# Kernel tuning notes

Hardware: AMD Instinct MI355X
Metric: run time of the kernel (lower is better)

## Reference

```python
import jax, jax.numpy as jnp
import numpy as np

EMB = 1024
NH = 16
T = 2048
B = 2

def setup_inputs() -> dict:
    key = jax.random.key(0)
    k1, k2, k3, k4, k5 = jax.random.split(key, 5)
    s = 0.02
    return {
        "x": jax.random.normal(k1, (B, T, EMB), dtype=jnp.float32),
        "W_attn": jax.random.normal(k2, (EMB, 3 * EMB), dtype=jnp.float32) * s,
        "b_attn": jax.random.normal(k3, (3 * EMB,), dtype=jnp.float32) * s,
        "W_proj": jax.random.normal(k4, (EMB, EMB), dtype=jnp.float32) * s,
        "b_proj": jax.random.normal(k5, (EMB,), dtype=jnp.float32) * s,
    }

def reference(x, W_attn, b_attn, W_proj, b_proj):
    Bz, Tz, C = x.shape
    hd = C // NH
    qkv = x @ W_attn + b_attn                      # [B,T,3C]
    q, k, v = jnp.split(qkv, 3, axis=-1)
    # [B,T,C] -> [B,H,T,hd]
    def heads(t):
        return t.reshape(Bz, Tz, NH, hd).transpose(0, 2, 1, 3)
    q, k, v = heads(q), heads(k), heads(v)
    scale = 1.0 / jnp.sqrt(jnp.float32(hd))
    att = jnp.einsum("bhqd,bhkd->bhqk", q, k) * scale   # [B,H,T,T]
    causal = jnp.tril(jnp.ones((Tz, Tz), dtype=bool))
    att = jnp.where(causal, att, jnp.finfo(att.dtype).min)
    att = jax.nn.softmax(att, axis=-1)
    y = jnp.einsum("bhqk,bhkd->bhqd", att, v)            # [B,H,T,hd]
    y = y.transpose(0, 2, 1, 3).reshape(Bz, Tz, C)
    return y @ W_proj + b_proj
```

## Files before the change

### kernel.cpp

```cpp
#include <hip/hip_runtime.h>
#include <cstdint>
#include <cstddef>

typedef _Float16 half8 __attribute__((ext_vector_type(8)));
typedef _Float16 half4v __attribute__((ext_vector_type(4)));
typedef float f32x4 __attribute__((ext_vector_type(4)));
typedef int int4v __attribute__((ext_vector_type(4)));

#define EMBD 1024
#define NHEAD 16
#define TSEQ 2048
#define NB 2
#define HD 64
#define NBH (NB*NHEAD)
#define SCK 0.18033688f

static __device__ __forceinline__ void gload_lds16(const void* g, void* l) {
    __builtin_amdgcn_global_load_lds((const __attribute__((address_space(1))) void*)g,
                                     (__attribute__((address_space(3))) void*)l,
                                     16, 0, 0);
}

static __device__ __forceinline__ int pk2(float a, float b) {
    return __builtin_bit_cast(int, __builtin_amdgcn_cvt_pkrtz(a, b));
}

__global__ __launch_bounds__(256) void k_prep(
    const float* __restrict__ x,  _Float16* __restrict__ xh,
    const float* __restrict__ Wa, const float* __restrict__ Wp,
    _Float16* __restrict__ WaT,   _Float16* __restrict__ WpT)
{
    const int bx = blockIdx.x;
    if (bx < 4096) {
        int i = bx * 256 + threadIdx.x;
        float4 v = ((const float4*)x)[i];
        half4v h;
        h.x = (_Float16)v.x; h.y = (_Float16)v.y; h.z = (_Float16)v.z; h.w = (_Float16)v.w;
        ((half4v*)xh)[i] = h;
        return;
    }
    __shared__ float tile[32][33];
    const int idx = bx - 4096;
    const int bxx = idx & 127;
    const int byy = idx >> 7;
    const bool isA = bxx < 96;
    const float* in  = isA ? Wa : Wp;
    _Float16* out    = isA ? WaT : WpT;
    const int C      = isA ? 3072 : 1024;
    const int c0 = (isA ? bxx : bxx - 96) * 32, r0 = byy * 32;
    const int tx = threadIdx.x & 31, ty = threadIdx.x >> 5;
    #pragma unroll
    for (int j = 0; j < 4; ++j)
        tile[ty + 8*j][tx] = in[(size_t)(r0 + ty + 8*j) * C + c0 + tx];
    __syncthreads();
    #pragma unroll
    for (int j = 0; j < 4; ++j)
        out[(size_t)(c0 + ty + 8*j) * 1024 + r0 + tx] = (_Float16)tile[tx][ty + 8*j];
}

__global__ __launch_bounds__(512, 4) void k_gemm_qkv(
    const _Float16* __restrict__ A,
    const _Float16* __restrict__ Bt,
    const float* __restrict__ bias,
    _Float16* __restrict__ outq,
    _Float16* __restrict__ VT)
{
    __shared__ _Float16 smem[20480];
    _Float16* As = smem;

    const int d   = blockIdx.x;
    const int xcd = d & 7;
    const int idx = d >> 3;
    const int mt  = (xcd >> 1) * 8 + (idx & 7);
    const int ntl = (xcd &  1) * 8 + (idx >> 3);
    const int m0 = mt * 128;
    const int hc = ntl * 64;

    const int tid  = threadIdx.x;
    const int lane = tid & 63;
    const int w    = tid >> 6;
    const int wm   = w >> 2;
    const int wn   = w & 3;
    const int l15  = lane & 15;
    const int lg   = lane >> 4;

    f32x4 acc[4][3];
    #pragma unroll
    for (int i = 0; i < 4; ++i)
        #pragma unroll
        for (int j = 0; j < 3; ++j)
            acc[i][j] = (f32x4){0.f, 0.f, 0.f, 0.f};

    for (int kt = 0; kt < 16; ++kt) {
        __syncthreads();
        #pragma unroll
        for (int c = 0; c < 2; ++c) {
            int s = c * 512 + tid;
            int r = s >> 3, sl = s & 7;
            const _Float16* ga = A + (size_t)(m0 + r) * 1024 + kt * 64 + ((sl ^ (r & 7)) * 8);
            gload_lds16(ga, (char*)As + s * 16);
        }
        {
            int s = tid;
            int r = s >> 3, sl = s & 7;
            size_t goff = (size_t)(hc + r) * 1024 + kt * 64 + ((sl ^ (r & 7)) * 8);
            #pragma unroll
            for (int q = 0; q < 3; ++q)
                gload_lds16(Bt + goff + (size_t)q * 1024 * 1024,
                            (char*)(smem + 8192 + q * 4096) + s * 16);
        }
        __syncthreads();

        half8 af[4][2];
        #pragma unroll
        for (int mf = 0; mf < 4; ++mf) {
            int r = wm * 64 + mf * 16 + l15;
            #pragma unroll
            for (int ks = 0; ks < 2; ++ks)
                af[mf][ks] = *(const half8*)((const char*)As + r * 128 + (((ks * 4 + lg) ^ (r & 7)) * 16));
        }
        half8 bf[3][2];
        #pragma unroll
        for (int nf = 0; nf < 3; ++nf) {
            int nn = wn * 48 + nf * 16;
            const char* BsQ = (const char*)(smem + 8192 + (nn >> 6) * 4096);
            int r = (nn & 63) + l15;
            #pragma unroll
            for (int ks = 0; ks < 2; ++ks)
                bf[nf][ks] = *(const half8*)(BsQ + r * 128 + (((ks * 4 + lg) ^ (r & 7)) * 16));
        }
        #pragma unroll
        for (int mf = 0; mf < 4; ++mf)
            #pragma unroll
            for (int nf = 0; nf < 3; ++nf) {
                acc[mf][nf] = __builtin_amdgcn_mfma_f32_16x16x32_f16(af[mf][0], bf[nf][0], acc[mf][nf], 0, 0, 0);
                acc[mf][nf] = __builtin_amdgcn_mfma_f32_16x16x32_f16(af[mf][1], bf[nf][1], acc[mf][nf], 0, 0, 0);
            }
    }

    #pragma unroll
    for (int nf = 0; nf < 3; ++nf) {
        int nn = wn * 48 + nf * 16;
        int q  = nn >> 6;
        if (q < 2) {
            int col = (nn & 63) + l15;
            float bv = bias[q * 1024 + hc + col];
            float osc = (q == 1) ? SCK : 1.0f;
            #pragma unroll
            for (int mf = 0; mf < 4; ++mf) {
                #pragma unroll
                for (int j = 0; j < 4; ++j) {
                    int m = m0 + wm * 64 + mf * 16 + lg * 4 + j;
                    outq[(size_t)m * 3072 + q * 1024 + hc + col] = (_Float16)((acc[mf][nf][j] + bv) * osc);
                }
            }
        }
    }
    __syncthreads();
    #pragma unroll
    for (int nf = 0; nf < 3; ++nf) {
        int nn = wn * 48 + nf * 16;
        if ((nn >> 6) == 2) {
            int col = (nn & 63) + l15;
            float bv = bias[2048 + hc + col];
            #pragma unroll
            for (int mf = 0; mf < 4; ++mf) {
                #pragma unroll
                for (int j = 0; j < 4; ++j) {
                    int ml = wm * 64 + mf * 16 + lg * 4 + j;
                    smem[ml * 65 + col] = (_Float16)(acc[mf][nf][j] + bv);
                }
            }
        }
    }
    __syncthreads();

    {
        const int b     = m0 >> 11;
        const int tloc0 = m0 & 2047;
        _Float16* vbase = VT + ((size_t)(b * 16 + ntl) * 64) * 2048 + tloc0;
        #pragma unroll
        for (int c = 0; c < 2; ++c) {
            int seg = c * 512 + tid;
            int dd  = seg >> 4;
            int s   = seg & 15;
            half8 hv8;
            #pragma unroll
            for (int e = 0; e < 8; ++e) {
                int p = s * 8 + e;
                int k = 16 * (2 * (p >> 5) + ((p & 7) >> 2)) + 4 * ((p >> 3) & 3) + (p & 3);
                hv8[e] = smem[k * 65 + dd];
            }
            *(half8*)&vbase[(size_t)dd * 2048 + s * 8] = hv8;
        }
    }
}

__global__ __launch_bounds__(256) void k_gemm_proj(
    const _Float16* __restrict__ A,
    const _Float16* __restrict__ Bt,
    const float* __restrict__ bias,
    float* __restrict__ outf)
{
    __shared__ _Float16 As[64 * 64];
    __shared__ _Float16 Bs[128 * 64];

    const int d   = blockIdx.x;
    const int xcd = d & 7;
    const int idx = d >> 3;
    const int mt  = (xcd >> 1) * 16 + (idx & 15);
    const int nt  = (xcd &  1) * 4  + (idx >> 4);
    const int m0 = mt * 64, n0 = nt * 128;

    const int tid  = threadIdx.x;
    const int lane = tid & 63;
    const int wn   = tid >> 6;
    const int l15  = lane & 15;
    const int lg   = lane >> 4;

    f32x4 acc[4][2];
    #pragma unroll
    for (int i = 0; i < 4; ++i) {
        acc[i][0] = (f32x4){0.f, 0.f, 0.f, 0.f};
        acc[i][1] = (f32x4){0.f, 0.f, 0.f, 0.f};
    }

    for (int kt = 0; kt < 16; ++kt) {
        __syncthreads();
        #pragma unroll
        for (int c = 0; c < 2; ++c) {
            int s = c * 256 + tid;
            int r = s >> 3, sl = s & 7;
            const _Float16* ga = A + (size_t)(m0 + r) * 1024 + kt * 64 + ((sl ^ (r & 7)) * 8);
            gload_lds16(ga, (char*)As + s * 16);
        }
        #pragma unroll
        for (int c = 0; c < 4; ++c) {
            int s = c * 256 + tid;
            int r = s >> 3, sl = s & 7;
            const _Float16* gb = Bt + (size_t)(n0 + r) * 1024 + kt * 64 + ((sl ^ (r & 7)) * 8);
            gload_lds16(gb, (char*)Bs + s * 16);
        }
        __syncthreads();

        half8 af[4][2], bf[2][2];
        #pragma unroll
        for (int mf = 0; mf < 4; ++mf) {
            int r = mf * 16 + l15;
            #pragma unroll
            for (int ks = 0; ks < 2; ++ks)
                af[mf][ks] = *(const half8*)((const char*)As + r * 128 + (((ks * 4 + lg) ^ (r & 7)) * 16));
        }
        #pragma unroll
        for (int nf = 0; nf < 2; ++nf) {
            int r = wn * 32 + nf * 16 + l15;
            #pragma unroll
            for (int ks = 0; ks < 2; ++ks)
                bf[nf][ks] = *(const half8*)((const char*)Bs + r * 128 + (((ks * 4 + lg) ^ (r & 7)) * 16));
        }
        #pragma unroll
        for (int mf = 0; mf < 4; ++mf)
            #pragma unroll
            for (int nf = 0; nf < 2; ++nf) {
                acc[mf][nf] = __builtin_amdgcn_mfma_f32_16x16x32_f16(af[mf][0], bf[nf][0], acc[mf][nf], 0, 0, 0);
                acc[mf][nf] = __builtin_amdgcn_mfma_f32_16x16x32_f16(af[mf][1], bf[nf][1], acc[mf][nf], 0, 0, 0);
            }
    }

    float bv[2];
    bv[0] = bias[n0 + wn * 32 + l15];
    bv[1] = bias[n0 + wn * 32 + 16 + l15];

    #pragma unroll
    for (int mf = 0; mf < 4; ++mf) {
        #pragma unroll
        for (int j = 0; j < 4; ++j) {
            int m = m0 + mf * 16 + lg * 4 + j;
            float* po = outf + (size_t)m * 1024 + n0 + wn * 32 + l15;
            po[0]  = acc[mf][0][j] + bv[0];
            po[16] = acc[mf][1][j] + bv[1];
        }
    }
}

__global__ __launch_bounds__(512) void k_attn(
    const _Float16* __restrict__ qkv,
    const _Float16* __restrict__ VTg,
    _Float16* __restrict__ Y)
{
    __shared__ _Float16 Kt[2][8192];
    __shared__ _Float16 Vt[2][8192];

    const int tid  = threadIdx.x;
    const int lane = tid & 63;
    const int w    = tid >> 6;
    const int l15  = lane & 15;
    const int lg   = lane >> 4;
    const int bh   = blockIdx.x;
    const int by   = blockIdx.y;
    const int qt   = (by < 8) ? (15 - by) : (by - 8);
    const int b    = bh >> 4, h = bh & 15;

    const int rA  = tid >> 3;
    const int slA = tid & 7;
    const size_t kOffA = (size_t)rA * 3072 + ((slA ^ (rA & 7)) * 8);
    const _Float16* kBase = qkv + (size_t)(b * 2048) * 3072 + 1024 + h * 64;

    const int dA = tid >> 4;
    const int sA = tid & 15;
    const size_t vOffA = (size_t)dA * 2048 + ((sA ^ (dA & 15)) * 8);
    const _Float16* vBase = VTg + (size_t)bh * TSEQ * HD;

    const int x7   = l15 & 7;
    const int kph0 = (lg ^ x7) * 8;
    const int kph1 = ((4 + lg) ^ x7) * 8;

    const int qrow = qt * 128 + w * 16 + l15;
    const _Float16* qptr = qkv + (size_t)(b * 2048 + qrow) * 3072 + h * 64;
    half8 qa0 = *(const half8*)&qptr[lg * 8];
    half8 qa1 = *(const half8*)&qptr[32 + lg * 8];

    half8 ones;
    #pragma unroll
    for (int i = 0; i < 8; ++i) ones[i] = (_Float16)1.0f;

    f32x4 yac[4];
    #pragma unroll
    for (int nf = 0; nf < 4; ++nf) yac[nf] = (f32x4){0.f, 0.f, 0.f, 0.f};
    f32x4 lsum = (f32x4){0.f, 0.f, 0.f, 0.f};

    const int nkt = qt + 1;

    half8 kra = *(const half8*)(kBase + kOffA);
    half8 krb = *(const half8*)(kBase + kOffA + (size_t)64 * 3072);
    half8 vra = *(const half8*)(vBase + vOffA);
    half8 vrb = *(const half8*)(vBase + vOffA + 32 * 2048);

    for (int kt = 0; kt < nkt; ++kt) {
        const int cur = kt & 1;
        _Float16* KtC = Kt[cur];
        _Float16* VtC = Vt[cur];
        *(half8*)&KtC[tid * 8]        = kra;
        *(half8*)&KtC[4096 + tid * 8] = krb;
        *(half8*)&VtC[tid * 8]        = vra;
        *(half8*)&VtC[4096 + tid * 8] = vrb;
        if (kt + 1 < nkt) {
            const _Float16* kp = kBase + (size_t)(kt + 1) * 128 * 3072;
            kra = *(const half8*)(kp + kOffA);
            krb = *(const half8*)(kp + kOffA + (size_t)64 * 3072);
            const _Float16* vp = vBase + (kt + 1) * 128;
            vra = *(const half8*)(vp + vOffA);
            vrb = *(const half8*)(vp + vOffA + 32 * 2048);
        }
        asm volatile("s_waitcnt lgkmcnt(0)" ::: "memory");
        __builtin_amdgcn_s_barrier();
        __builtin_amdgcn_sched_barrier(0);

        const bool diag = (kt == nkt - 1);

        f32x4 s[8];
        __builtin_amdgcn_s_setprio(1);
        #pragma unroll
        for (int f = 0; f < 8; ++f) {
            if (diag && f > w) { s[f] = (f32x4){0.f, 0.f, 0.f, 0.f}; continue; }
            int rr = f * 16 + l15;
            half8 kb0 = *(const half8*)&KtC[rr * 64 + kph0];
            half8 kb1 = *(const half8*)&KtC[rr * 64 + kph1];
            f32x4 z = (f32x4){0.f, 0.f, 0.f, 0.f};
            z = __builtin_amdgcn_mfma_f32_16x16x32_f16(kb0, qa0, z, 0, 0, 0);
            z = __builtin_amdgcn_mfma_f32_16x16x32_f16(kb1, qa1, z, 0, 0, 0);
            s[f] = z;
        }
        __builtin_amdgcn_s_setprio(0);

        if (diag) {
            const int qg = qt * 128 + w * 16 + l15;
            #pragma unroll
            for (int f = 0; f < 8; ++f) {
                if (f > w) continue;
                #pragma unroll
                for (int j = 0; j < 4; ++j) {
                    int kk = kt * 128 + 16 * f + 4 * lg + j;
                    s[f][j] = (kk > qg) ? 0.f : exp2f(s[f][j]);
                }
            }
        } else {
            #pragma unroll
            for (int f = 0; f < 8; ++f)
                #pragma unroll
                for (int j = 0; j < 4; ++j) s[f][j] = exp2f(s[f][j]);
        }

        __builtin_amdgcn_s_setprio(1);
        #pragma unroll
        for (int t = 0; t < 4; ++t) {
            int4v pi;
            pi[0] = pk2(s[2 * t][0],     s[2 * t][1]);
            pi[1] = pk2(s[2 * t][2],     s[2 * t][3]);
            pi[2] = pk2(s[2 * t + 1][0], s[2 * t + 1][1]);
            pi[3] = pk2(s[2 * t + 1][2], s[2 * t + 1][3]);
            half8 pa = __builtin_bit_cast(half8, pi);
            lsum = __builtin_amdgcn_mfma_f32_16x16x32_f16(pa, ones, lsum, 0, 0, 0);
            #pragma unroll
            for (int nf = 0; nf < 4; ++nf) {
                half8 vb = *(const half8*)&VtC[(nf * 16 + l15) * 128 + (((t * 4 + lg) ^ l15) * 8)];
                yac[nf] = __builtin_amdgcn_mfma_f32_16x16x32_f16(pa, vb, yac[nf], 0, 0, 0);
            }
        }
        __builtin_amdgcn_s_setprio(0);
    }

    const int trow = qt * 128 + w * 16 + lg * 4;
    #pragma unroll
    for (int j = 0; j < 4; ++j) {
        float inv = 1.f / lsum[j];
        #pragma unroll
        for (int nf = 0; nf < 4; ++nf) {
            float yv = yac[nf][j] * inv;
            Y[((size_t)b * TSEQ + trow + j) * EMBD + h * 64 + nf * 16 + l15] = (_Float16)yv;
        }
    }
}

extern "C" void kernel_launch(void* const* d_in, const int* in_sizes, int n_in,
                              void* d_out, int out_size, void* d_ws, size_t ws_size,
                              hipStream_t stream) {
    const float* x  = (const float*)d_in[0];
    const float* Wa = (const float*)d_in[1];
    const float* ba = (const float*)d_in[2];
    const float* Wp = (const float*)d_in[3];
    const float* bp = (const float*)d_in[4];
    float* out = (float*)d_out;

    _Float16* Xh   = (_Float16*)d_ws;
    _Float16* WaT  = Xh   + (size_t)4096 * 1024;
    _Float16* WpT  = WaT  + (size_t)3072 * 1024;
    _Float16* QKVn = WpT  + (size_t)1024 * 1024;
    _Float16* VTb  = QKVn + (size_t)4096 * 3072;
    _Float16* Yh   = Xh;

    k_prep<<<8192, 256, 0, stream>>>(x, Xh, Wa, Wp, WaT, WpT);

    k_gemm_qkv<<<512, 512, 0, stream>>>(Xh, WaT, ba, QKVn, VTb);

    k_attn<<<dim3(NBH, 16), 512, 0, stream>>>(QKVn, VTb, Yh);

    k_gemm_proj<<<512, 256, 0, stream>>>(Yh, WpT, bp, out);
}
```

Before: 91.70 us.

## Halve attention block to 4 waves, each handling two 16-row query slices

The attention kernel now runs 256 threads per block instead of 512. Each wave processes two 16-row query fragments (rows w*16 and w*16+64) that share every K and V fragment loaded from LDS, so LDS read traffic per MFMA halves and each thread stages four K/V chunks instead of two. The diagonal-tile skip for fully masked fragments is dropped, so masked blocks are computed and then zeroed. The changes also raise register pressure, with launch bounds asking for two blocks per CU, and cut the number of waves available to hide latency.

```diff
diff --git a/kernel.cpp b/kernel.cpp
--- a/kernel.cpp
+++ b/kernel.cpp
@@ -283,7 +283,7 @@
     }
 }
 
-__global__ __launch_bounds__(512) void k_attn(
+__global__ __launch_bounds__(256, 2) void k_attn(
     const _Float16* __restrict__ qkv,
     const _Float16* __restrict__ VTg,
     _Float16* __restrict__ Y)
@@ -301,110 +301,145 @@
     const int qt   = (by < 8) ? (15 - by) : (by - 8);
     const int b    = bh >> 4, h = bh & 15;
 
-    const int rA  = tid >> 3;
-    const int slA = tid & 7;
-    const size_t kOffA = (size_t)rA * 3072 + ((slA ^ (rA & 7)) * 8);
+    const int sg0 = tid, sg1 = 256 + tid, sg2 = 512 + tid, sg3 = 768 + tid;
+    const size_t k0 = (size_t)(sg0 >> 3) * 3072 + (((sg0 & 7) ^ ((sg0 >> 3) & 7)) * 8);
+    const size_t k1 = (size_t)(sg1 >> 3) * 3072 + (((sg1 & 7) ^ ((sg1 >> 3) & 7)) * 8);
+    const size_t k2 = (size_t)(sg2 >> 3) * 3072 + (((sg2 & 7) ^ ((sg2 >> 3) & 7)) * 8);
+    const size_t k3 = (size_t)(sg3 >> 3) * 3072 + (((sg3 & 7) ^ ((sg3 >> 3) & 7)) * 8);
+    const size_t v0 = (size_t)(sg0 >> 4) * 2048 + (((sg0 & 15) ^ ((sg0 >> 4) & 15)) * 8);
+    const size_t v1 = (size_t)(sg1 >> 4) * 2048 + (((sg1 & 15) ^ ((sg1 >> 4) & 15)) * 8);
+    const size_t v2 = (size_t)(sg2 >> 4) * 2048 + (((sg2 & 15) ^ ((sg2 >> 4) & 15)) * 8);
+    const size_t v3 = (size_t)(sg3 >> 4) * 2048 + (((sg3 & 15) ^ ((sg3 >> 4) & 15)) * 8);
     const _Float16* kBase = qkv + (size_t)(b * 2048) * 3072 + 1024 + h * 64;
-
-    const int dA = tid >> 4;
-    const int sA = tid & 15;
-    const size_t vOffA = (size_t)dA * 2048 + ((sA ^ (dA & 15)) * 8);
     const _Float16* vBase = VTg + (size_t)bh * TSEQ * HD;
 
     const int x7   = l15 & 7;
     const int kph0 = (lg ^ x7) * 8;
     const int kph1 = ((4 + lg) ^ x7) * 8;
 
-    const int qrow = qt * 128 + w * 16 + l15;
-    const _Float16* qptr = qkv + (size_t)(b * 2048 + qrow) * 3072 + h * 64;
-    half8 qa0 = *(const half8*)&qptr[lg * 8];
-    half8 qa1 = *(const half8*)&qptr[32 + lg * 8];
+    const int qr0 = qt * 128 + w * 16 + l15;
+    const _Float16* qp0 = qkv + (size_t)(b * 2048 + qr0) * 3072 + h * 64;
+    const _Float16* qp1 = qp0 + (size_t)64 * 3072;
+    half8 qa0 = *(const half8*)&qp0[lg * 8];
+    half8 qa1 = *(const half8*)&qp0[32 + lg * 8];
+    half8 qa2 = *(const half8*)&qp1[lg * 8];
+    half8 qa3 = *(const half8*)&qp1[32 + lg * 8];
 
     half8 ones;
     #pragma unroll
     for (int i = 0; i < 8; ++i) ones[i] = (_Float16)1.0f;
 
-    f32x4 yac[4];
-    #pragma unroll
-    for (int nf = 0; nf < 4; ++nf) yac[nf] = (f32x4){0.f, 0.f, 0.f, 0.f};
-    f32x4 lsum = (f32x4){0.f, 0.f, 0.f, 0.f};
+    f32x4 yac0[4], yac1[4];
+    #pragma unroll
+    for (int nf = 0; nf < 4; ++nf) {
+        yac0[nf] = (f32x4){0.f, 0.f, 0.f, 0.f};
+        yac1[nf] = (f32x4){0.f, 0.f, 0.f, 0.f};
+    }
+    f32x4 lsum0 = (f32x4){0.f, 0.f, 0.f, 0.f};
+    f32x4 lsum1 = (f32x4){0.f, 0.f, 0.f, 0.f};
 
     const int nkt = qt + 1;
-
-    half8 kra = *(const half8*)(kBase + kOffA);
-    half8 krb = *(const half8*)(kBase + kOffA + (size_t)64 * 3072);
-    half8 vra = *(const half8*)(vBase + vOffA);
-    half8 vrb = *(const half8*)(vBase + vOffA + 32 * 2048);
+    const int qg0 = qt * 128 + w * 16 + l15;
+    const int qg1 = qg0 + 64;
+
+    half8 kra0 = *(const half8*)(kBase + k0);
+    half8 kra1 = *(const half8*)(kBase + k1);
+    half8 kra2 = *(const half8*)(kBase + k2);
+    half8 kra3 = *(const half8*)(kBase + k3);
+    half8 vra0 = *(const half8*)(vBase + v0);
+    half8 vra1 = *(const half8*)(vBase + v1);
+    half8 vra2 = *(const half8*)(vBase + v2);
+    half8 vra3 = *(const half8*)(vBase + v3);
 
     for (int kt = 0; kt < nkt; ++kt) {
         const int cur = kt & 1;
         _Float16* KtC = Kt[cur];
         _Float16* VtC = Vt[cur];
-        *(half8*)&KtC[tid * 8]        = kra;
-        *(half8*)&KtC[4096 + tid * 8] = krb;
-        *(half8*)&VtC[tid * 8]        = vra;
-        *(half8*)&VtC[4096 + tid * 8] = vrb;
+        *(half8*)&KtC[sg0 * 8] = kra0;
+        *(half8*)&KtC[sg1 * 8] = kra1;
+        *(half8*)&KtC[sg2 * 8] = kra2;
+        *(half8*)&KtC[sg3 * 8] = kra3;
+        *(half8*)&VtC[sg0 * 8] = vra0;
+        *(half8*)&VtC[sg1 * 8] = vra1;
+        *(half8*)&VtC[sg2 * 8] = vra2;
+        *(half8*)&VtC[sg3 * 8] = vra3;
         if (kt + 1 < nkt) {
             const _Float16* kp = kBase + (size_t)(kt + 1) * 128 * 3072;
-            kra = *(const half8*)(kp + kOffA);
-            krb = *(const half8*)(kp + kOffA + (size_t)64 * 3072);
-            const _Float16* vp = vBase + (kt + 1) * 128;
-            vra = *(const half8*)(vp + vOffA);
-            vrb = *(const half8*)(vp + vOffA + 32 * 2048);
+            const _Float16* vp = vBase + (size_t)(kt + 1) * 128;
+            kra0 = *(const half8*)(kp + k0);
+            kra1 = *(const half8*)(kp + k1);
+            kra2 = *(const half8*)(kp + k2);
+            kra3 = *(const half8*)(kp + k3);
+            vra0 = *(const half8*)(vp + v0);
+            vra1 = *(const half8*)(vp + v1);
+            vra2 = *(const half8*)(vp + v2);
+            vra3 = *(const half8*)(vp + v3);
         }
         asm volatile("s_waitcnt lgkmcnt(0)" ::: "memory");
         __builtin_amdgcn_s_barrier();
         __builtin_amdgcn_sched_barrier(0);
 
         const bool diag = (kt == nkt - 1);
-
-        f32x4 s[8];
+        const int kb0g  = kt * 128;
+
+        f32x4 s0[8], s1[8];
         __builtin_amdgcn_s_setprio(1);
         #pragma unroll
         for (int f = 0; f < 8; ++f) {
-            if (diag && f > w) { s[f] = (f32x4){0.f, 0.f, 0.f, 0.f}; continue; }
             int rr = f * 16 + l15;
             half8 kb0 = *(const half8*)&KtC[rr * 64 + kph0];
             half8 kb1 = *(const half8*)&KtC[rr * 64 + kph1];
-            f32x4 z = (f32x4){0.f, 0.f, 0.f, 0.f};
-            z = __builtin_amdgcn_mfma_f32_16x16x32_f16(kb0, qa0, z, 0, 0, 0);
-            z = __builtin_amdgcn_mfma_f32_16x16x32_f16(kb1, qa1, z, 0, 0, 0);
-            s[f] = z;
+            f32x4 z0 = (f32x4){0.f, 0.f, 0.f, 0.f};
+            f32x4 z1 = (f32x4){0.f, 0.f, 0.f, 0.f};
+            z0 = __builtin_amdgcn_mfma_f32_16x16x32_f16(kb0, qa0, z0, 0, 0, 0);
+            z0 = __builtin_amdgcn_mfma_f32_16x16x32_f16(kb1, qa1, z0, 0, 0, 0);
+            z1 = __builtin_amdgcn_mfma_f32_16x16x32_f16(kb0, qa2, z1, 0, 0, 0);
+            z1 = __builtin_amdgcn_mfma_f32_16x16x32_f16(kb1, qa3, z1, 0, 0, 0);
+            s0[f] = z0;
+            s1[f] = z1;
         }
         __builtin_amdgcn_s_setprio(0);
 
         if (diag) {
-            const int qg = qt * 128 + w * 16 + l15;
-            #pragma unroll
-            for (int f = 0; f < 8; ++f) {
-                if (f > w) continue;
+            #pragma unroll
+            for (int f = 0; f < 8; ++f)
                 #pragma unroll
                 for (int j = 0; j < 4; ++j) {
-                    int kk = kt * 128 + 16 * f + 4 * lg + j;
-                    s[f][j] = (kk > qg) ? 0.f : exp2f(s[f][j]);
+                    int kk = kb0g + 16 * f + 4 * lg + j;
+                    s0[f][j] = (kk > qg0) ? 0.f : exp2f(s0[f][j]);
+                    s1[f][j] = (kk > qg1) ? 0.f : exp2f(s1[f][j]);
                 }
-            }
         } else {
             #pragma unroll
             for (int f = 0; f < 8; ++f)
                 #pragma unroll
-                for (int j = 0; j < 4; ++j) s[f][j] = exp2f(s[f][j]);
+                for (int j = 0; j < 4; ++j) {
+                    s0[f][j] = exp2f(s0[f][j]);
+                    s1[f][j] = exp2f(s1[f][j]);
+                }
         }
 
         __builtin_amdgcn_s_setprio(1);
         #pragma unroll
         for (int t = 0; t < 4; ++t) {
-            int4v pi;
-            pi[0] = pk2(s[2 * t][0],     s[2 * t][1]);
-            pi[1] = pk2(s[2 * t][2],     s[2 * t][3]);
-            pi[2] = pk2(s[2 * t + 1][0], s[2 * t + 1][1]);
-            pi[3] = pk2(s[2 * t + 1][2], s[2 * t + 1][3]);
-            half8 pa = __builtin_bit_cast(half8, pi);
-            lsum = __builtin_amdgcn_mfma_f32_16x16x32_f16(pa, ones, lsum, 0, 0, 0);
+            int4v pi0, pi1;
+            pi0[0] = pk2(s0[2 * t][0],     s0[2 * t][1]);
+            pi0[1] = pk2(s0[2 * t][2],     s0[2 * t][3]);
+            pi0[2] = pk2(s0[2 * t + 1][0], s0[2 * t + 1][1]);
+            pi0[3] = pk2(s0[2 * t + 1][2], s0[2 * t + 1][3]);
+            pi1[0] = pk2(s1[2 * t][0],     s1[2 * t][1]);
+            pi1[1] = pk2(s1[2 * t][2],     s1[2 * t][3]);
+            pi1[2] = pk2(s1[2 * t + 1][0], s1[2 * t + 1][1]);
+            pi1[3] = pk2(s1[2 * t + 1][2], s1[2 * t + 1][3]);
+            half8 pa0 = __builtin_bit_cast(half8, pi0);
+            half8 pa1 = __builtin_bit_cast(half8, pi1);
+            lsum0 = __builtin_amdgcn_mfma_f32_16x16x32_f16(pa0, ones, lsum0, 0, 0, 0);
+            lsum1 = __builtin_amdgcn_mfma_f32_16x16x32_f16(pa1, ones, lsum1, 0, 0, 0);
             #pragma unroll
             for (int nf = 0; nf < 4; ++nf) {
                 half8 vb = *(const half8*)&VtC[(nf * 16 + l15) * 128 + (((t * 4 + lg) ^ l15) * 8)];
-                yac[nf] = __builtin_amdgcn_mfma_f32_16x16x32_f16(pa, vb, yac[nf], 0, 0, 0);
+                yac0[nf] = __builtin_amdgcn_mfma_f32_16x16x32_f16(pa0, vb, yac0[nf], 0, 0, 0);
+                yac1[nf] = __builtin_amdgcn_mfma_f32_16x16x32_f16(pa1, vb, yac1[nf], 0, 0, 0);
             }
         }
         __builtin_amdgcn_s_setprio(0);
@@ -413,11 +448,14 @@
     const int trow = qt * 128 + w * 16 + lg * 4;
     #pragma unroll
     for (int j = 0; j < 4; ++j) {
-        float inv = 1.f / lsum[j];
+        float inv0 = 1.f / lsum0[j];
+        float inv1 = 1.f / lsum1[j];
         #pragma unroll
         for (int nf = 0; nf < 4; ++nf) {
-            float yv = yac[nf][j] * inv;
-            Y[((size_t)b * TSEQ + trow + j) * EMBD + h * 64 + nf * 16 + l15] = (_Float16)yv;
+            Y[((size_t)b * TSEQ + trow + j) * EMBD + h * 64 + nf * 16 + l15]
+                = (_Float16)(yac0[nf][j] * inv0);
+            Y[((size_t)b * TSEQ + trow + 64 + j) * EMBD + h * 64 + nf * 16 + l15]
+                = (_Float16)(yac1[nf][j] * inv1);
         }
     }
 }
@@ -443,7 +481,7 @@
 
     k_gemm_qkv<<<512, 512, 0, stream>>>(Xh, WaT, ba, QKVn, VTb);
 
-    k_attn<<<dim3(NBH, 16), 512, 0, stream>>>(QKVn, VTb, Yh);
+    k_attn<<<dim3(NBH, 16), 256, 0, stream>>>(QKVn, VTb, Yh);
 
     k_gemm_proj<<<512, 256, 0, stream>>>(Yh, WpT, bp, out);
 }
```

After: 92.93 us. About the same (+1.3%).
